# Performance work log

Measured on AMD Instinct MI355X. Metric: run time of the kernel, lower is better.

Reference implementation:

```python
import jax, jax.numpy as jnp
import numpy as np

N, E, D = 100000, 1600000, 128
BN_EPS = 1e-5


def setup_inputs() -> dict:
    key = jax.random.key(0)
    k0, k1, k2 = jax.random.split(key, 3)
    x = jax.random.normal(k0, (N, D), dtype=jnp.float32)
    edge_index = jax.random.randint(k1, (2, E), 0, N, dtype=jnp.int32)
    # GCNConv weight (glorot-ish scale) and bias
    W = jax.random.normal(k2, (D, D), dtype=jnp.float32) * (1.0 / np.sqrt(D))
    b = jnp.zeros((D,), dtype=jnp.float32)
    # BatchNorm1d affine params
    gamma = jnp.ones((D,), dtype=jnp.float32)
    beta = jnp.zeros((D,), dtype=jnp.float32)
    # PReLU single shared slope (torch default init 0.25)
    a_prelu = jnp.asarray(0.25, dtype=jnp.float32)
    return {"x": x, "W": W, "b": b, "gamma": gamma, "beta": beta,
            "a_prelu": a_prelu, "edge_index": edge_index}


def reference(x, W, b, gamma, beta, a_prelu, edge_index):
    n = x.shape[0]
    loops = jnp.arange(n, dtype=edge_index.dtype)
    src = jnp.concatenate([edge_index[0], loops])  # [E+N]
    dst = jnp.concatenate([edge_index[1], loops])  # [E+N]

    # GCN symmetric normalization with self-loops: deg counts incoming edges
    deg = jax.ops.segment_sum(jnp.ones_like(dst, dtype=x.dtype), dst, num_segments=n)
    dinv = jax.lax.rsqrt(deg)  # deg >= 1 thanks to self-loops
    enorm = dinv[src] * dinv[dst]  # [E+N]

    xw = x @ W                                        # [N, D] transform first
    msg = xw[src] * enorm[:, None]                    # gather + scale
    out = jax.ops.segment_sum(msg, dst, num_segments=n) + b  # scatter-add

    # BatchNorm1d over nodes (training-mode batch statistics, biased var)
    mean = jnp.mean(out, axis=0)
    var = jnp.mean(jnp.square(out - mean), axis=0)
    out = (out - mean) * jax.lax.rsqrt(var + BN_EPS) * gamma + beta

    # PReLU (single shared slope); dropout is identity in eval mode
    out = jnp.where(out > 0, out, a_prelu * out)

    # identity residual (in_dim == out_dim)
    return out + x
```

## Files before the change

### kernel.cpp

```cpp
#include <hip/hip_runtime.h>

#define DIM 128
#define BSH 8
#define BUCK 256
#define CAP 6144
#define BINCH 2048
#define MAXB 1024

typedef __attribute__((ext_vector_type(8))) short bf16x8;
typedef __attribute__((ext_vector_type(4))) float f32x4;
union U8 { uint4 u; bf16x8 b; };

static __device__ __forceinline__ unsigned f2bf_bits(float f) {
  unsigned u = __float_as_uint(f);
  return (u + 0x7fffu + ((u >> 16) & 1u)) >> 16;
}
static __device__ __forceinline__ unsigned packbf(float a, float b) {
  return (f2bf_bits(a) & 0xffffu) | (f2bf_bits(b) << 16);
}
static __device__ __forceinline__ float bfu_lo(unsigned pk) { return __uint_as_float(pk << 16); }
static __device__ __forceinline__ float bfu_hi(unsigned pk) { return __uint_as_float(pk & 0xffff0000u); }

static __device__ __forceinline__ int eread(const int* __restrict__ e, long long idx, int fl64) {
  return fl64 ? e[idx * 2] : e[idx];
}

__global__ void k_probe(const int* __restrict__ eidx, int* __restrict__ iflag) {
  int lane = threadIdx.x;
  int w = eidx[lane * 2 + 1];
  unsigned long long m = __ballot(w == 0);
  if (lane == 0) *iflag = (__popcll(m) >= 48) ? 1 : 0;
}

__global__ __launch_bounds__(256) void k_prep(const int* __restrict__ eidx, int E,
                                              const int* __restrict__ iflag,
                                              int* __restrict__ bcnt,
                                              unsigned* __restrict__ tmp, int nbuck,
                                              const float* __restrict__ x,
                                              unsigned* __restrict__ xb, int n,
                                              const float* __restrict__ W,
                                              unsigned* __restrict__ wbt,
                                              int NBB, int NWT) {
  __shared__ int hist[MAXB];
  __shared__ int lcur[MAXB];
  int bid = blockIdx.x;
  int tid = threadIdx.x;

  if (bid < NBB) {
    int fl = *iflag;
    long long ebase = (long long)bid * BINCH;
    for (int i = tid; i < nbuck; i += 256) hist[i] = 0;
    __syncthreads();
    unsigned pk[BINCH / 256];
    int bb[BINCH / 256];
#pragma unroll
    for (int it = 0; it < BINCH / 256; ++it) {
      long long e = ebase + it * 256 + tid;
      bb[it] = -1;
      if (e < E) {
        int s = eread(eidx, e, fl);
        int d = eread(eidx, (long long)E + e, fl);
        bb[it] = d >> BSH;
        pk[it] = ((unsigned)s << BSH) | (unsigned)(d & (BUCK - 1));
        atomicAdd(&hist[bb[it]], 1);
      }
    }
    __syncthreads();
    for (int b = tid; b < nbuck; b += 256) {
      int h = hist[b];
      lcur[b] = h ? atomicAdd(&bcnt[b], h) : 0;
    }
    __syncthreads();
#pragma unroll
    for (int it = 0; it < BINCH / 256; ++it) {
      if (bb[it] >= 0) {
        int sl = atomicAdd(&lcur[bb[it]], 1);
        if (sl < CAP) tmp[(unsigned)bb[it] * CAP + sl] = pk[it];
      }
    }
  } else if (bid < NBB + NWT) {
    int w = (bid - NBB) * 256 + tid;
    int c = w >> 6, kk = w & 63;
    float lo = W[(unsigned)(2 * kk) * DIM + c];
    float hi = W[(unsigned)(2 * kk + 1) * DIM + c];
    wbt[(unsigned)c * 64 + kk] = packbf(lo, hi);
  } else {
    int t = (bid - NBB - NWT) * 256 + tid;
    int i = t >> 6, p = t & 63;
    if (i >= n) return;
    float2 v = *(const float2*)(x + (size_t)i * DIM + p * 2);
    xb[(unsigned)i * 64 + p] = packbf(v.x, v.y);
  }
}

__global__ __launch_bounds__(512) void k_fine(const int* __restrict__ bcnt,
                                              unsigned* __restrict__ tmp,
                                              int* __restrict__ ofs2,
                                              int* __restrict__ deg,
                                              float* __restrict__ dinv, int n) {
  __shared__ unsigned raw[CAP];
  __shared__ unsigned srt[CAP];
  __shared__ int hist[BUCK];
  __shared__ int sc[BUCK];
  __shared__ int lcur[BUCK];
  int b = blockIdx.x, tid = threadIdx.x;
  int cnt = bcnt[b];
  if (cnt > CAP) cnt = CAP;
  unsigned base = (unsigned)b * CAP;
  if (tid < BUCK) hist[tid] = 0;
  __syncthreads();
  for (int j = tid; j < cnt; j += 512) {
    unsigned pk = tmp[base + j];
    raw[j] = pk;
    atomicAdd(&hist[pk & (BUCK - 1)], 1);
  }
  __syncthreads();
  int v = 0;
  if (tid < BUCK) {
    v = hist[tid];
    sc[tid] = v;
  }
  __syncthreads();
  for (int d = 1; d < BUCK; d <<= 1) {
    int t = (tid < BUCK && tid >= d) ? sc[tid - d] : 0;
    __syncthreads();
    if (tid < BUCK) sc[tid] += t;
    __syncthreads();
  }
  int excl = 0;
  if (tid < BUCK) {
    excl = sc[tid] - v;
    lcur[tid] = excl;
  }
  __syncthreads();
  for (int j = tid; j < cnt; j += 512) {
    unsigned pk = raw[j];
    int sl = atomicAdd(&lcur[pk & (BUCK - 1)], 1);
    srt[sl] = pk;
  }
  __syncthreads();
  for (int j = tid; j < cnt; j += 512) tmp[base + j] = srt[j];
  int node = b * BUCK + tid;
  if (tid < BUCK && node < n) {
    ofs2[node] = (int)base + excl;
    deg[node] = v;
    dinv[node] = rsqrtf((float)(v + 1));
  }
}

__global__ __launch_bounds__(256) void k_agg(const unsigned* __restrict__ xb,
                                             const unsigned* __restrict__ tmp,
                                             const int* __restrict__ ofs2,
                                             const int* __restrict__ deg,
                                             const float* __restrict__ dinv,
                                             unsigned* __restrict__ agg, int n) {
  int wid = blockIdx.x * 4 + (threadIdx.x >> 6);
  int lane = threadIdx.x & 63;
  if (wid >= n) return;
  float di = dinv[wid];
  unsigned xp = xb[(unsigned)wid * 64 + lane];
  float ax = bfu_lo(xp) * di, ay = bfu_hi(xp) * di;
  int e = ofs2[wid], e1 = e + deg[wid];
  if ((e & 1) && e < e1) {
    unsigned k = tmp[(unsigned)e];
    unsigned s = k >> BSH;
    unsigned vv = xb[s * 64 + lane];
    float w = dinv[s];
    ax = fmaf(w, bfu_lo(vv), ax); ay = fmaf(w, bfu_hi(vv), ay);
    ++e;
  }
  for (; e + 8 <= e1; e += 8) {
    uint2 q0 = *(const uint2*)&tmp[(unsigned)e];
    uint2 q1 = *(const uint2*)&tmp[(unsigned)e + 2];
    uint2 q2 = *(const uint2*)&tmp[(unsigned)e + 4];
    uint2 q3 = *(const uint2*)&tmp[(unsigned)e + 6];
    unsigned s0 = q0.x >> BSH, s1 = q0.y >> BSH, s2 = q1.x >> BSH, s3 = q1.y >> BSH;
    unsigned s4 = q2.x >> BSH, s5 = q2.y >> BSH, s6 = q3.x >> BSH, s7 = q3.y >> BSH;
    unsigned v0 = xb[s0 * 64 + lane], v1 = xb[s1 * 64 + lane];
    unsigned v2 = xb[s2 * 64 + lane], v3 = xb[s3 * 64 + lane];
    unsigned v4 = xb[s4 * 64 + lane], v5 = xb[s5 * 64 + lane];
    unsigned v6 = xb[s6 * 64 + lane], v7 = xb[s7 * 64 + lane];
    float w0 = dinv[s0], w1 = dinv[s1], w2 = dinv[s2], w3 = dinv[s3];
    float w4 = dinv[s4], w5 = dinv[s5], w6 = dinv[s6], w7 = dinv[s7];
    ax = fmaf(w0, bfu_lo(v0), ax); ay = fmaf(w0, bfu_hi(v0), ay);
    ax = fmaf(w1, bfu_lo(v1), ax); ay = fmaf(w1, bfu_hi(v1), ay);
    ax = fmaf(w2, bfu_lo(v2), ax); ay = fmaf(w2, bfu_hi(v2), ay);
    ax = fmaf(w3, bfu_lo(v3), ax); ay = fmaf(w3, bfu_hi(v3), ay);
    ax = fmaf(w4, bfu_lo(v4), ax); ay = fmaf(w4, bfu_hi(v4), ay);
    ax = fmaf(w5, bfu_lo(v5), ax); ay = fmaf(w5, bfu_hi(v5), ay);
    ax = fmaf(w6, bfu_lo(v6), ax); ay = fmaf(w6, bfu_hi(v6), ay);
    ax = fmaf(w7, bfu_lo(v7), ax); ay = fmaf(w7, bfu_hi(v7), ay);
  }
  for (; e + 2 <= e1; e += 2) {
    uint2 q = *(const uint2*)&tmp[(unsigned)e];
    unsigned s0 = q.x >> BSH, s1 = q.y >> BSH;
    unsigned v0 = xb[s0 * 64 + lane], v1 = xb[s1 * 64 + lane];
    float w0 = dinv[s0], w1 = dinv[s1];
    ax = fmaf(w0, bfu_lo(v0), ax); ay = fmaf(w0, bfu_hi(v0), ay);
    ax = fmaf(w1, bfu_lo(v1), ax); ay = fmaf(w1, bfu_hi(v1), ay);
  }
  if (e < e1) {
    unsigned k = tmp[(unsigned)e];
    unsigned s = k >> BSH;
    unsigned vv = xb[s * 64 + lane];
    float w = dinv[s];
    ax = fmaf(w, bfu_lo(vv), ax); ay = fmaf(w, bfu_hi(vv), ay);
  }
  agg[(unsigned)wid * 64 + lane] = packbf(ax * di, ay * di);
}

__global__ __launch_bounds__(256) void k_gemm(
    const unsigned* __restrict__ agg, const unsigned* __restrict__ wbt,
    const float* __restrict__ bias, unsigned* __restrict__ preb,
    float* __restrict__ part, int n) {
  __shared__ unsigned SM[64 * 68 + 128 * 68];
  unsigned* As2 = SM;
  unsigned* WsT = SM + 64 * 68;
  int tid = threadIdx.x;
  int base = blockIdx.x * 64;

#pragma unroll
  for (int it = 0; it < 32; ++it) {
    int idx = it * 256 + tid;
    int c = idx >> 6, kk = idx & 63;
    WsT[c * 68 + kk] = wbt[idx];
  }
#pragma unroll
  for (int it = 0; it < 16; ++it) {
    int idx = it * 256 + tid;
    int rl = idx >> 6, c2 = idx & 63;
    int g = base + rl; if (g >= n) g = n - 1;
    As2[rl * 68 + c2] = agg[(unsigned)g * 64 + c2];
  }
  __syncthreads();

  int w = tid >> 6, l = tid & 63;
  int lg = l >> 4, lr = l & 15;
  f32x4 acc[8];
#pragma unroll
  for (int nt = 0; nt < 8; ++nt) acc[nt] = (f32x4){0.f, 0.f, 0.f, 0.f};

#pragma unroll
  for (int kt = 0; kt < 4; ++kt) {
    U8 bfr;
    bfr.u = *(const uint4*)&As2[(w * 16 + lr) * 68 + kt * 16 + lg * 4];
#pragma unroll
    for (int nt = 0; nt < 8; ++nt) {
      U8 afr;
      afr.u = *(const uint4*)&WsT[(nt * 16 + lr) * 68 + kt * 16 + lg * 4];
      acc[nt] = __builtin_amdgcn_mfma_f32_16x16x32_bf16(afr.b, bfr.b, acc[nt], 0, 0, 0);
    }
  }
  __syncthreads();

  float* Cf = (float*)SM;
#pragma unroll
  for (int nt = 0; nt < 8; ++nt) {
    *(f32x4*)&Cf[(w * 16 + lr) * 132 + nt * 16 + lg * 4] = acc[nt];
  }
  __syncthreads();

  float* bn = Cf + 64 * 132;
  int c2 = tid & 63, g4 = tid >> 6;
  float b0 = bias[2 * c2], b1 = bias[2 * c2 + 1];
  float cs0 = 0.f, cs1 = 0.f, cq0 = 0.f, cq1 = 0.f;
#pragma unroll
  for (int it = 0; it < 16; ++it) {
    int m = it * 4 + g4;
    int gg = base + m;
    float2 vv = *(const float2*)&Cf[m * 132 + 2 * c2];
    float v0 = vv.x + b0, v1 = vv.y + b1;
    if (gg < n) {
      preb[(unsigned)gg * 64 + c2] = packbf(v0, v1);
      cs0 += v0; cq0 += v0 * v0;
      cs1 += v1; cq1 += v1 * v1;
    }
  }
  bn[g4 * 256 + 2 * c2] = cs0;
  bn[g4 * 256 + 2 * c2 + 1] = cs1;
  bn[g4 * 256 + 128 + 2 * c2] = cq0;
  bn[g4 * 256 + 128 + 2 * c2 + 1] = cq1;
  __syncthreads();
  part[(size_t)blockIdx.x * 256 + tid] = bn[tid] + bn[256 + tid] + bn[512 + tid] + bn[768 + tid];
}

__global__ __launch_bounds__(256) void k_redbn(const float* __restrict__ part, int nb,
                                               const float* __restrict__ gma,
                                               const float* __restrict__ bta,
                                               float* __restrict__ sc_,
                                               float* __restrict__ sh_, float invn) {
  __shared__ float r1[256], r2[256];
  int c = blockIdx.x, t = threadIdx.x;
  float s = 0.f, q = 0.f;
  for (int i = t; i < nb; i += 256) {
    s += part[(size_t)i * 256 + c];
    q += part[(size_t)i * 256 + 128 + c];
  }
  r1[t] = s; r2[t] = q;
  __syncthreads();
  for (int k = 128; k > 0; k >>= 1) {
    if (t < k) { r1[t] += r1[t + k]; r2[t] += r2[t + k]; }
    __syncthreads();
  }
  if (t == 0) {
    float mean = r1[0] * invn;
    float var = r2[0] * invn - mean * mean;
    float inv = rsqrtf(var + 1e-5f);
    float g = gma[c] * inv;
    sc_[c] = g;
    sh_[c] = bta[c] - mean * g;
  }
}

__global__ __launch_bounds__(256) void k_final(const unsigned* __restrict__ preb,
                                               const float* __restrict__ x,
                                               const float* __restrict__ sc,
                                               const float* __restrict__ sh,
                                               const float* __restrict__ apre,
                                               float* __restrict__ out, int n) {
  int t = blockIdx.x * 256 + threadIdx.x;
  int i = t >> 6, p = t & 63;
  if (i >= n) return;
  float a = apre[0];
  int c = p * 2;
  unsigned pk = preb[(unsigned)i * 64 + p];
  float t0 = bfu_lo(pk) * sc[c] + sh[c];
  float t1 = bfu_hi(pk) * sc[c + 1] + sh[c + 1];
  t0 = t0 > 0.f ? t0 : a * t0;
  t1 = t1 > 0.f ? t1 : a * t1;
  float2 xv = *(const float2*)(x + (size_t)i * DIM + c);
  t0 += xv.x;
  t1 += xv.y;
  *(float2*)(out + (size_t)i * DIM + c) = make_float2(t0, t1);
}

extern "C" void kernel_launch(void* const* d_in, const int* in_sizes, int n_in,
                              void* d_out, int out_size, void* d_ws, size_t ws_size,
                              hipStream_t stream) {
  (void)n_in; (void)out_size; (void)ws_size;
  const float* x    = (const float*)d_in[0];
  const float* W    = (const float*)d_in[1];
  const float* b    = (const float*)d_in[2];
  const float* gma  = (const float*)d_in[3];
  const float* bta  = (const float*)d_in[4];
  const float* apre = (const float*)d_in[5];
  const int* eidx   = (const int*)d_in[6];
  float* out        = (float*)d_out;

  const int N = in_sizes[0] / DIM;
  const int E = in_sizes[6] / 2;
  const int NB = (N + 63) / 64;
  const int NBUCK = (N + BUCK - 1) / BUCK;
  const int NBB = (E + BINCH - 1) / BINCH;
  const int NWT = 32;
  const int NPK = (N * 64 + 255) / 256;

  char* wsb = (char*)d_ws;
  size_t off_b = 0;
  auto take = [&](size_t bytes) -> void* {
    void* p = wsb + off_b;
    off_b += (bytes + 255) & ~(size_t)255;
    return p;
  };
  int*      iflag = (int*)     take(256);
  int*      deg   = (int*)     take((size_t)N * 4);
  int*      bcnt  = (int*)     take((size_t)NBUCK * 4);
  int*      ofs2  = (int*)     take((size_t)N * 4);
  float*    dinv  = (float*)   take((size_t)N * 4);
  unsigned* wbt   = (unsigned*)take((size_t)DIM * 64 * 4);
  unsigned* tmp   = (unsigned*)take((size_t)NBUCK * CAP * 4);
  unsigned* xb    = (unsigned*)take((size_t)N * 64 * 4);
  unsigned* agg   = (unsigned*)take((size_t)N * 64 * 4);
  float*    part  = (float*)   take((size_t)NB * 256 * 4);
  float*    sc    = (float*)   take(DIM * 4);
  float*    sh    = (float*)   take(DIM * 4);
  unsigned* preb  = agg;

  hipMemsetAsync(bcnt, 0, (size_t)NBUCK * 4, stream);

  k_probe <<<1, 64, 0, stream>>>(eidx, iflag);
  k_prep  <<<NBB + NWT + NPK, 256, 0, stream>>>(eidx, E, iflag, bcnt, tmp, NBUCK,
                                                x, xb, N, W, wbt, NBB, NWT);
  k_fine  <<<NBUCK, 512, 0, stream>>>(bcnt, tmp, ofs2, deg, dinv, N);
  k_agg   <<<(N + 3) / 4, 256, 0, stream>>>(xb, tmp, ofs2, deg, dinv, agg, N);
  k_gemm  <<<NB, 256, 0, stream>>>(agg, wbt, b, preb, part, N);
  k_redbn <<<DIM, 256, 0, stream>>>(part, NB, gma, bta, sc, sh, 1.0f / (float)N);
  k_final <<<(N * 64 + 255) / 256, 256, 0, stream>>>(preb, x, sc, sh, apre, out, N);
}
```

Baseline: 262.3 us.

## Prescale packed features by dinv, simplify aggregation gather, register-resident fine sort

```diff
diff --git a/kernel.cpp b/kernel.cpp
--- a/kernel.cpp
+++ b/kernel.cpp
@@ -4,8 +4,9 @@
 #define BSH 8
 #define BUCK 256
 #define CAP 6144
-#define BINCH 2048
+#define BINCH 1024
 #define MAXB 1024
+#define FPT 12
 
 typedef __attribute__((ext_vector_type(8))) short bf16x8;
 typedef __attribute__((ext_vector_type(4))) float f32x4;
@@ -36,11 +37,9 @@
                                               const int* __restrict__ iflag,
                                               int* __restrict__ bcnt,
                                               unsigned* __restrict__ tmp, int nbuck,
-                                              const float* __restrict__ x,
-                                              unsigned* __restrict__ xb, int n,
                                               const float* __restrict__ W,
                                               unsigned* __restrict__ wbt,
-                                              int NBB, int NWT) {
+                                              int NBB) {
   __shared__ int hist[MAXB];
   __shared__ int lcur[MAXB];
   int bid = blockIdx.x;
@@ -78,18 +77,12 @@
         if (sl < CAP) tmp[(unsigned)bb[it] * CAP + sl] = pk[it];
       }
     }
-  } else if (bid < NBB + NWT) {
+  } else {
     int w = (bid - NBB) * 256 + tid;
     int c = w >> 6, kk = w & 63;
     float lo = W[(unsigned)(2 * kk) * DIM + c];
     float hi = W[(unsigned)(2 * kk + 1) * DIM + c];
     wbt[(unsigned)c * 64 + kk] = packbf(lo, hi);
-  } else {
-    int t = (bid - NBB - NWT) * 256 + tid;
-    int i = t >> 6, p = t & 63;
-    if (i >= n) return;
-    float2 v = *(const float2*)(x + (size_t)i * DIM + p * 2);
-    xb[(unsigned)i * 64 + p] = packbf(v.x, v.y);
   }
 }
 
@@ -98,7 +91,6 @@
                                               int* __restrict__ ofs2,
                                               int* __restrict__ deg,
                                               float* __restrict__ dinv, int n) {
-  __shared__ unsigned raw[CAP];
   __shared__ unsigned srt[CAP];
   __shared__ int hist[BUCK];
   __shared__ int sc[BUCK];
@@ -109,43 +101,68 @@
   unsigned base = (unsigned)b * CAP;
   if (tid < BUCK) hist[tid] = 0;
   __syncthreads();
-  for (int j = tid; j < cnt; j += 512) {
-    unsigned pk = tmp[base + j];
-    raw[j] = pk;
-    atomicAdd(&hist[pk & (BUCK - 1)], 1);
-  }
-  __syncthreads();
-  int v = 0;
+  unsigned r[FPT];
+#pragma unroll
+  for (int u = 0; u < FPT; ++u) {
+    int j = u * 512 + tid;
+    r[u] = 0xffffffffu;
+    if (j < cnt) {
+      r[u] = tmp[base + j];
+      atomicAdd(&hist[r[u] & (BUCK - 1)], 1);
+    }
+  }
+  __syncthreads();
+  if (tid < 64) {
+    int h0 = hist[tid * 4], h1 = hist[tid * 4 + 1];
+    int h2 = hist[tid * 4 + 2], h3 = hist[tid * 4 + 3];
+    int s = h0 + h1 + h2 + h3;
+    int pre = s;
+#pragma unroll
+    for (int d = 1; d < 64; d <<= 1) {
+      int t = __shfl_up(pre, d);
+      if (tid >= d) pre += t;
+    }
+    pre -= s;
+    int e0 = pre, e1 = pre + h0, e2 = e1 + h1, e3 = e2 + h2;
+    sc[tid * 4] = e0;     lcur[tid * 4] = e0;
+    sc[tid * 4 + 1] = e1; lcur[tid * 4 + 1] = e1;
+    sc[tid * 4 + 2] = e2; lcur[tid * 4 + 2] = e2;
+    sc[tid * 4 + 3] = e3; lcur[tid * 4 + 3] = e3;
+  }
+  __syncthreads();
+#pragma unroll
+  for (int u = 0; u < FPT; ++u) {
+    if (r[u] != 0xffffffffu) {
+      int sl = atomicAdd(&lcur[r[u] & (BUCK - 1)], 1);
+      srt[sl] = r[u];
+    }
+  }
+  __syncthreads();
+#pragma unroll
+  for (int u = 0; u < FPT; ++u) {
+    int j = u * 512 + tid;
+    if (j < cnt) tmp[base + j] = srt[j];
+  }
   if (tid < BUCK) {
-    v = hist[tid];
-    sc[tid] = v;
-  }
-  __syncthreads();
-  for (int d = 1; d < BUCK; d <<= 1) {
-    int t = (tid < BUCK && tid >= d) ? sc[tid - d] : 0;
-    __syncthreads();
-    if (tid < BUCK) sc[tid] += t;
-    __syncthreads();
-  }
-  int excl = 0;
-  if (tid < BUCK) {
-    excl = sc[tid] - v;
-    lcur[tid] = excl;
-  }
-  __syncthreads();
-  for (int j = tid; j < cnt; j += 512) {
-    unsigned pk = raw[j];
-    int sl = atomicAdd(&lcur[pk & (BUCK - 1)], 1);
-    srt[sl] = pk;
-  }
-  __syncthreads();
-  for (int j = tid; j < cnt; j += 512) tmp[base + j] = srt[j];
-  int node = b * BUCK + tid;
-  if (tid < BUCK && node < n) {
-    ofs2[node] = (int)base + excl;
-    deg[node] = v;
-    dinv[node] = rsqrtf((float)(v + 1));
-  }
+    int node = b * BUCK + tid;
+    if (node < n) {
+      int v = hist[tid];
+      ofs2[node] = (int)base + sc[tid];
+      deg[node] = v;
+      dinv[node] = rsqrtf((float)(v + 1));
+    }
+  }
+}
+
+__global__ __launch_bounds__(256) void k_pack(const float* __restrict__ x,
+                                              const float* __restrict__ dinv,
+                                              unsigned* __restrict__ xb, int n) {
+  int t = blockIdx.x * 256 + threadIdx.x;
+  int i = t >> 6, p = t & 63;
+  if (i >= n) return;
+  float di = dinv[i];
+  float2 v = *(const float2*)(x + (size_t)i * DIM + p * 2);
+  xb[(unsigned)i * 64 + p] = packbf(v.x * di, v.y * di);
 }
 
 __global__ __launch_bounds__(256) void k_agg(const unsigned* __restrict__ xb,
@@ -159,52 +176,32 @@
   if (wid >= n) return;
   float di = dinv[wid];
   unsigned xp = xb[(unsigned)wid * 64 + lane];
-  float ax = bfu_lo(xp) * di, ay = bfu_hi(xp) * di;
-  int e = ofs2[wid], e1 = e + deg[wid];
-  if ((e & 1) && e < e1) {
-    unsigned k = tmp[(unsigned)e];
-    unsigned s = k >> BSH;
-    unsigned vv = xb[s * 64 + lane];
-    float w = dinv[s];
-    ax = fmaf(w, bfu_lo(vv), ax); ay = fmaf(w, bfu_hi(vv), ay);
-    ++e;
-  }
-  for (; e + 8 <= e1; e += 8) {
-    uint2 q0 = *(const uint2*)&tmp[(unsigned)e];
-    uint2 q1 = *(const uint2*)&tmp[(unsigned)e + 2];
-    uint2 q2 = *(const uint2*)&tmp[(unsigned)e + 4];
-    uint2 q3 = *(const uint2*)&tmp[(unsigned)e + 6];
-    unsigned s0 = q0.x >> BSH, s1 = q0.y >> BSH, s2 = q1.x >> BSH, s3 = q1.y >> BSH;
-    unsigned s4 = q2.x >> BSH, s5 = q2.y >> BSH, s6 = q3.x >> BSH, s7 = q3.y >> BSH;
+  float ax = bfu_lo(xp), ay = bfu_hi(xp);
+  int e = __builtin_amdgcn_readfirstlane(ofs2[wid]);
+  int e1 = e + __builtin_amdgcn_readfirstlane(deg[wid]);
+  for (; e + 16 <= e1; e += 16) {
+    unsigned s[16];
+#pragma unroll
+    for (int u = 0; u < 16; ++u) s[u] = tmp[(unsigned)(e + u)] >> BSH;
+    unsigned v[16];
+#pragma unroll
+    for (int u = 0; u < 16; ++u) v[u] = xb[s[u] * 64 + lane];
+#pragma unroll
+    for (int u = 0; u < 16; ++u) { ax += bfu_lo(v[u]); ay += bfu_hi(v[u]); }
+  }
+  for (; e + 4 <= e1; e += 4) {
+    unsigned s0 = tmp[(unsigned)e] >> BSH, s1 = tmp[(unsigned)e + 1] >> BSH;
+    unsigned s2 = tmp[(unsigned)e + 2] >> BSH, s3 = tmp[(unsigned)e + 3] >> BSH;
     unsigned v0 = xb[s0 * 64 + lane], v1 = xb[s1 * 64 + lane];
     unsigned v2 = xb[s2 * 64 + lane], v3 = xb[s3 * 64 + lane];
-    unsigned v4 = xb[s4 * 64 + lane], v5 = xb[s5 * 64 + lane];
-    unsigned v6 = xb[s6 * 64 + lane], v7 = xb[s7 * 64 + lane];
-    float w0 = dinv[s0], w1 = dinv[s1], w2 = dinv[s2], w3 = dinv[s3];
-    float w4 = dinv[s4], w5 = dinv[s5], w6 = dinv[s6], w7 = dinv[s7];
-    ax = fmaf(w0, bfu_lo(v0), ax); ay = fmaf(w0, bfu_hi(v0), ay);
-    ax = fmaf(w1, bfu_lo(v1), ax); ay = fmaf(w1, bfu_hi(v1), ay);
-    ax = fmaf(w2, bfu_lo(v2), ax); ay = fmaf(w2, bfu_hi(v2), ay);
-    ax = fmaf(w3, bfu_lo(v3), ax); ay = fmaf(w3, bfu_hi(v3), ay);
-    ax = fmaf(w4, bfu_lo(v4), ax); ay = fmaf(w4, bfu_hi(v4), ay);
-    ax = fmaf(w5, bfu_lo(v5), ax); ay = fmaf(w5, bfu_hi(v5), ay);
-    ax = fmaf(w6, bfu_lo(v6), ax); ay = fmaf(w6, bfu_hi(v6), ay);
-    ax = fmaf(w7, bfu_lo(v7), ax); ay = fmaf(w7, bfu_hi(v7), ay);
-  }
-  for (; e + 2 <= e1; e += 2) {
-    uint2 q = *(const uint2*)&tmp[(unsigned)e];
-    unsigned s0 = q.x >> BSH, s1 = q.y >> BSH;
-    unsigned v0 = xb[s0 * 64 + lane], v1 = xb[s1 * 64 + lane];
-    float w0 = dinv[s0], w1 = dinv[s1];
-    ax = fmaf(w0, bfu_lo(v0), ax); ay = fmaf(w0, bfu_hi(v0), ay);
-    ax = fmaf(w1, bfu_lo(v1), ax); ay = fmaf(w1, bfu_hi(v1), ay);
-  }
-  if (e < e1) {
-    unsigned k = tmp[(unsigned)e];
-    unsigned s = k >> BSH;
-    unsigned vv = xb[s * 64 + lane];
-    float w = dinv[s];
-    ax = fmaf(w, bfu_lo(vv), ax); ay = fmaf(w, bfu_hi(vv), ay);
+    ax += bfu_lo(v0); ay += bfu_hi(v0);
+    ax += bfu_lo(v1); ay += bfu_hi(v1);
+    ax += bfu_lo(v2); ay += bfu_hi(v2);
+    ax += bfu_lo(v3); ay += bfu_hi(v3);
+  }
+  for (; e < e1; ++e) {
+    unsigned vv = xb[(tmp[(unsigned)e] >> BSH) * 64 + lane];
+    ax += bfu_lo(vv); ay += bfu_hi(vv);
   }
   agg[(unsigned)wid * 64 + lane] = packbf(ax * di, ay * di);
 }
@@ -353,7 +350,6 @@
   const int NBUCK = (N + BUCK - 1) / BUCK;
   const int NBB = (E + BINCH - 1) / BINCH;
   const int NWT = 32;
-  const int NPK = (N * 64 + 255) / 256;
 
   char* wsb = (char*)d_ws;
   size_t off_b = 0;
@@ -379,9 +375,9 @@
   hipMemsetAsync(bcnt, 0, (size_t)NBUCK * 4, stream);
 
   k_probe <<<1, 64, 0, stream>>>(eidx, iflag);
-  k_prep  <<<NBB + NWT + NPK, 256, 0, stream>>>(eidx, E, iflag, bcnt, tmp, NBUCK,
-                                                x, xb, N, W, wbt, NBB, NWT);
+  k_prep  <<<NBB + NWT, 256, 0, stream>>>(eidx, E, iflag, bcnt, tmp, NBUCK, W, wbt, NBB);
   k_fine  <<<NBUCK, 512, 0, stream>>>(bcnt, tmp, ofs2, deg, dinv, N);
+  k_pack  <<<(N * 64 + 255) / 256, 256, 0, stream>>>(x, dinv, xb, N);
   k_agg   <<<(N + 3) / 4, 256, 0, stream>>>(xb, tmp, ofs2, deg, dinv, agg, N);
   k_gemm  <<<NB, 256, 0, stream>>>(agg, wbt, b, preb, part, N);
   k_redbn <<<DIM, 256, 0, stream>>>(part, NB, gma, bta, sc, sh, 1.0f / (float)N);
```

New measurement: 280.2 us. 6.9% more time.
